# Performance work log

Hardware: AMD Instinct MI355X
Metric: run time of the kernel (lower is better)

The kernel has to match this reference:

```python
import jax, jax.numpy as jnp
import numpy as np

N_USERS = 100000
M_ITEMS = 50000
EMBED = 64
N_LAYERS = 3
NNZ = 2400000
BATCH = 8192


def setup_inputs() -> dict:
    key = jax.random.key(0)
    ks = jax.random.split(key, 8)
    user = jax.random.randint(ks[0], (BATCH,), 0, N_USERS)
    item_i = jax.random.randint(ks[1], (BATCH,), 0, M_ITEMS)
    item_j = jax.random.randint(ks[2], (BATCH,), 0, M_ITEMS)
    timestamp = jax.random.uniform(ks[3], (BATCH,), dtype=jnp.float32)
    # symmetric bipartite edge list: user->item and item->user halves
    half = NNZ // 2
    u = jax.random.randint(ks[4], (half,), 0, N_USERS)
    it = jax.random.randint(ks[5], (half,), 0, M_ITEMS) + N_USERS
    edge_src = jnp.concatenate([u, it])
    edge_dst = jnp.concatenate([it, u])
    v = jax.random.uniform(ks[6], (half,), dtype=jnp.float32)
    edge_vals = jnp.concatenate([v, v])  # symmetric normalized weights
    embed_user_0 = jax.random.normal(ks[7], (N_USERS, EMBED), dtype=jnp.float32) * 0.1
    embed_item_0 = jax.random.normal(jax.random.fold_in(key, 99), (M_ITEMS, EMBED), dtype=jnp.float32) * 0.1
    return {
        'user': user, 'item_i': item_i, 'item_j': item_j,
        'timestamp': timestamp, 'split_idx': 0,
        'edge_src': edge_src, 'edge_dst': edge_dst, 'edge_vals': edge_vals,
        'embed_user_0': embed_user_0, 'embed_item_0': embed_item_0,
    }


def reference(user, item_i, item_j, timestamp, split_idx,
              edge_src, edge_dst, edge_vals, embed_user_0, embed_item_0):
    N = N_USERS + M_ITEMS
    # LightGCN propagation: mean over layer-0..n_layers embeddings
    all_emb = jnp.concatenate([embed_user_0, embed_item_0], axis=0)  # [N, D]
    emb = all_emb
    emb_sum = all_emb
    for _ in range(N_LAYERS):
        # sparse.mm(Graph, emb): gather source features along edges, scale, segment-reduce
        emb = jax.ops.segment_sum(edge_vals[:, None] * emb[edge_dst], edge_src,
                                  num_segments=N)
        emb_sum = emb_sum + emb
    light_out = emb_sum / (N_LAYERS + 1)
    embed_user = light_out[:N_USERS]
    embed_item = light_out[N_USERS:]

    ue = embed_user[user]          # [B, D]
    ie = embed_item[item_i]        # [B, D]
    je = embed_item[item_j]        # [B, D]
    prediction_i = jnp.sum(ue * ie, axis=-1)
    prediction_j = jnp.sum(ue * je, axis=-1)

    # reg_loss uses layer-0 embeddings gathered at the batch indices
    u0 = embed_user_0[user]
    i0 = embed_item_0[item_i]
    j0 = embed_item_0[item_j]
    reg_loss = 0.5 * (jnp.sum(u0 * u0) + jnp.sum(i0 * i0) + jnp.sum(j0 * j0)) / user.shape[0]
    return prediction_i, prediction_j, reg_loss
```

## Files before the change

### kernel.cpp

```cpp
#include <hip/hip_runtime.h>

#define N_USERS 100000
#define M_ITEMS 50000
#define NNODES  (N_USERS + M_ITEMS)
#define EMBED   64
#define N_LAYERS 3
#define BATCH   8192

#define NU_E ((size_t)N_USERS * EMBED)
#define NI_E ((size_t)M_ITEMS * EMBED)
#define NE   ((size_t)NNODES * EMBED)

#define NPB    256
#define NBUCK  ((NNODES + NPB - 1) / NPB)
#define PBLK   256
#define HBB_N  (NBUCK * PBLK)
#define DBINS  1024
#define NCH    256
#define CHUNK  ((NNODES + NCH - 1) / NCH)
#define HBN    (DBINS * NCH)
#define PRED_BLOCKS ((BATCH * 64) / 256)

typedef unsigned int uint;

static __device__ __forceinline__ ushort f2bf(float f) {
    uint u = __float_as_uint(f);
    return (ushort)((u + 0x7fffu + ((u >> 16) & 1u)) >> 16);
}
static __device__ __forceinline__ float bf_lo(uint u) { return __uint_as_float(u << 16); }
static __device__ __forceinline__ float bf_hi(uint u) { return __uint_as_float(u & 0xffff0000u); }
static __device__ __forceinline__ float bfs(ushort u) { return __uint_as_float((uint)u << 16); }

__global__ void init_emb(const float* __restrict__ eu, const float* __restrict__ ei,
                         ushort* __restrict__ E0) {
    size_t t = (size_t)blockIdx.x * blockDim.x + threadIdx.x;
    const size_t nu4 = NU_E / 4;
    const size_t n4  = NE / 4;
    if (t >= n4) return;
    float4 v = (t < nu4) ? ((const float4*)eu)[t] : ((const float4*)ei)[t - nu4];
    ((ushort4*)E0)[t] = make_ushort4(f2bf(v.x), f2bf(v.y), f2bf(v.z), f2bf(v.w));
}

__global__ void hist_pass(const int* __restrict__ src, int* __restrict__ Hbb,
                          int nnz, int tile) {
    __shared__ int h[NBUCK];
    for (int i = threadIdx.x; i < NBUCK; i += blockDim.x) h[i] = 0;
    __syncthreads();
    int base = blockIdx.x * tile;
    int end  = min(base + tile, nnz);
    for (int i = base + threadIdx.x; i < end; i += blockDim.x)
        atomicAdd(&h[src[i] >> 8], 1);
    __syncthreads();
    for (int i = threadIdx.x; i < NBUCK; i += blockDim.x)
        Hbb[i * PBLK + blockIdx.x] = h[i];
}

__global__ void scan_local(int* __restrict__ h, int* __restrict__ bsum, int n) {
    __shared__ int lds[256];
    const int tid = threadIdx.x;
    const int base = blockIdx.x * 1024 + tid * 4;
    int v[4]; int s = 0;
    #pragma unroll
    for (int c = 0; c < 4; ++c) { v[c] = (base + c < n) ? h[base + c] : 0; s += v[c]; }
    lds[tid] = s;
    __syncthreads();
    for (int off = 1; off < 256; off <<= 1) {
        int t = (tid >= off) ? lds[tid - off] : 0;
        __syncthreads();
        lds[tid] += t;
        __syncthreads();
    }
    if (tid == 255) bsum[blockIdx.x] = lds[255];
    int run = (tid > 0) ? lds[tid - 1] : 0;
    #pragma unroll
    for (int c = 0; c < 4; ++c) {
        int t = v[c];
        if (base + c < n) h[base + c] = run;
        run += t;
    }
}
__global__ void scan_bsums(int* __restrict__ bsum, int nblk) {
    __shared__ int lds[256];
    int tid = threadIdx.x;
    lds[tid] = (tid < nblk) ? bsum[tid] : 0;
    __syncthreads();
    for (int off = 1; off < 256; off <<= 1) {
        int t = (tid >= off) ? lds[tid - off] : 0;
        __syncthreads();
        lds[tid] += t;
        __syncthreads();
    }
    if (tid < nblk) bsum[tid] = (tid > 0) ? lds[tid - 1] : 0;
}
__global__ void scan_add(int* __restrict__ h, const int* __restrict__ bsum, int n) {
    int i = blockIdx.x * blockDim.x + threadIdx.x;
    if (i >= n) return;
    h[i] += bsum[i / 1024];
}

__global__ void partition2(const int* __restrict__ src, const int* __restrict__ dst,
                           const float* __restrict__ vals, const int* __restrict__ Hbb,
                           int2* __restrict__ ebuf, int nnz, int tile) {
    __shared__ int cur[NBUCK];
    for (int i = threadIdx.x; i < NBUCK; i += blockDim.x)
        cur[i] = Hbb[i * PBLK + blockIdx.x];
    __syncthreads();
    int base = blockIdx.x * tile;
    int end  = min(base + tile, nnz);
    for (int i = base + threadIdx.x; i < end; i += blockDim.x) {
        int s = src[i];
        int d = dst[i];
        float v = vals[i];
        if (d >= N_USERS) d -= N_USERS;
        int p = atomicAdd(&cur[s >> 8], 1);
        ebuf[p] = make_int2((s & 255) | (d << 8), __float_as_int(v));
    }
}

__global__ void bucket_sort(const int* __restrict__ Hbb, const int2* __restrict__ ebuf,
                            int* __restrict__ offs, int2* __restrict__ ep, int nnz) {
    __shared__ int cnt[256];
    __shared__ int sc[256];
    __shared__ int cur[256];
    int b   = blockIdx.x;
    int tid = threadIdx.x;
    int beg = Hbb[b * PBLK];
    int end = (b + 1 < NBUCK) ? Hbb[(b + 1) * PBLK] : nnz;
    if (tid < 256) cnt[tid] = 0;
    __syncthreads();
    for (int i = beg + tid; i < end; i += blockDim.x)
        atomicAdd(&cnt[ebuf[i].x & 255], 1);
    __syncthreads();
    if (tid < 256) sc[tid] = cnt[tid];
    __syncthreads();
    for (int off = 1; off < 256; off <<= 1) {
        int t = (tid >= off && tid < 256) ? sc[tid - off] : 0;
        __syncthreads();
        if (tid < 256) sc[tid] += t;
        __syncthreads();
    }
    if (tid < 256) {
        int nodeBase = beg + ((tid > 0) ? sc[tid - 1] : 0);
        int node = b * NPB + tid;
        if (node < NNODES) offs[node] = nodeBase;
        cur[tid] = nodeBase;
    }
    __syncthreads();
    for (int i = beg + tid; i < end; i += blockDim.x) {
        int2 e = ebuf[i];
        int p = atomicAdd(&cur[e.x & 255], 1);
        ep[p] = make_int2(e.x >> 8, e.y);
    }
    if (b == 0 && tid == 0) offs[NNODES] = nnz;
}

__global__ void deg_hist_blk(const int* __restrict__ offs, int* __restrict__ Hb) {
    __shared__ int h[DBINS];
    int blk = blockIdx.x;
    for (int i = threadIdx.x; i < DBINS; i += blockDim.x) h[i] = 0;
    __syncthreads();
    int base = blk * CHUNK, end = min(base + CHUNK, NNODES);
    for (int n = base + threadIdx.x; n < end; n += blockDim.x)
        atomicAdd(&h[min(offs[n + 1] - offs[n], DBINS - 1)], 1);
    __syncthreads();
    for (int i = threadIdx.x; i < DBINS; i += blockDim.x)
        Hb[i * NCH + blk] = h[i];
}
__global__ void deg_scatter_blk(const int* __restrict__ offs, const int* __restrict__ Hb,
                                int* __restrict__ perm) {
    __shared__ int cur[DBINS];
    int blk = blockIdx.x;
    for (int i = threadIdx.x; i < DBINS; i += blockDim.x)
        cur[i] = Hb[i * NCH + blk];
    __syncthreads();
    int base = blk * CHUNK, end = min(base + CHUNK, NNODES);
    for (int n = base + threadIdx.x; n < end; n += blockDim.x) {
        int d = min(offs[n + 1] - offs[n], DBINS - 1);
        int p = atomicAdd(&cur[d], 1);
        perm[p] = n;
    }
}

__global__ void gather_E(const int* __restrict__ offs, const int2* __restrict__ ep,
                         const int* __restrict__ perm,
                         const ushort* __restrict__ Eprev, ushort* __restrict__ Enext,
                         int nnz) {
    int t = blockIdx.x * blockDim.x + threadIdx.x;
    int wave = t >> 6;
    int lane = t & 63;
    int g = lane >> 3;
    int q = lane & 7;
    int ln = wave * 8 + g;
    bool valid = ln < NNODES;
    int node = valid ? perm[ln] : 0;
    int start = valid ? offs[node] : 0;
    int deg   = valid ? offs[node + 1] - start : 0;
    bool isUser = node < N_USERS;
    const uint4* other = (const uint4*)(Eprev + (isUser ? NU_E : 0));
    int lastIdx = min(max(start + deg - 1, 0), nnz - 1);

    int md = deg;
    #pragma unroll
    for (int off = 8; off <= 32; off <<= 1) md = max(md, __shfl_xor(md, off));

    float a0=0.f,a1=0.f,a2=0.f,a3=0.f,a4=0.f,a5=0.f,a6=0.f,a7=0.f;
    for (int k = 0; k < md; k += 8) {
        int2 e[8];
        uint4 r[8];
        #pragma unroll
        for (int c = 0; c < 8; ++c) {
            int idx = (k + c < deg) ? start + k + c : lastIdx;
            e[c] = ep[idx];
            if (k + c >= deg) e[c].y = 0;
        }
        #pragma unroll
        for (int c = 0; c < 8; ++c)
            r[c] = other[(size_t)e[c].x * 8 + q];
        #pragma unroll
        for (int c = 0; c < 8; ++c) {
            float v = __int_as_float(e[c].y);
            a0 = fmaf(v, bf_lo(r[c].x), a0);  a1 = fmaf(v, bf_hi(r[c].x), a1);
            a2 = fmaf(v, bf_lo(r[c].y), a2);  a3 = fmaf(v, bf_hi(r[c].y), a3);
            a4 = fmaf(v, bf_lo(r[c].z), a4);  a5 = fmaf(v, bf_hi(r[c].z), a5);
            a6 = fmaf(v, bf_lo(r[c].w), a6);  a7 = fmaf(v, bf_hi(r[c].w), a7);
        }
    }

    if (!valid) return;
    uint4 o;
    o.x = (uint)f2bf(a0) | ((uint)f2bf(a1) << 16);
    o.y = (uint)f2bf(a2) | ((uint)f2bf(a3) << 16);
    o.z = (uint)f2bf(a4) | ((uint)f2bf(a5) << 16);
    o.w = (uint)f2bf(a6) | ((uint)f2bf(a7) << 16);
    ((uint4*)Enext)[(size_t)node * 8 + q] = o;
}

__global__ void predict_kernel(const int* __restrict__ user, const int* __restrict__ item_i,
                               const int* __restrict__ item_j,
                               const ushort* __restrict__ E0, const ushort* __restrict__ E1,
                               const ushort* __restrict__ E2, const ushort* __restrict__ E3,
                               const float* __restrict__ eu0, const float* __restrict__ ei0,
                               float* __restrict__ out, float* __restrict__ rbuf) {
    __shared__ float rpart[4];
    int t = blockIdx.x * blockDim.x + threadIdx.x;
    int b = t >> 6;
    int d = t & 63;
    int wv = threadIdx.x >> 6;
    float pi = 0.f, pj = 0.f, r = 0.f;
    if (b < BATCH) {
        size_t ru = (size_t)user[b] * EMBED + d;
        size_t ri = ((size_t)N_USERS + item_i[b]) * EMBED + d;
        size_t rj = ((size_t)N_USERS + item_j[b]) * EMBED + d;
        float ue = bfs(E0[ru]) + bfs(E1[ru]) + bfs(E2[ru]) + bfs(E3[ru]);
        float ie = bfs(E0[ri]) + bfs(E1[ri]) + bfs(E2[ri]) + bfs(E3[ri]);
        float je = bfs(E0[rj]) + bfs(E1[rj]) + bfs(E2[rj]) + bfs(E3[rj]);
        pi = ue * ie;
        pj = ue * je;
        float u0 = eu0[(size_t)user[b] * EMBED + d];
        float i0 = ei0[(size_t)item_i[b] * EMBED + d];
        float j0 = ei0[(size_t)item_j[b] * EMBED + d];
        r = u0 * u0 + i0 * i0 + j0 * j0;
    }
    #pragma unroll
    for (int off = 32; off > 0; off >>= 1) {
        pi += __shfl_down(pi, off);
        pj += __shfl_down(pj, off);
        r  += __shfl_down(r,  off);
    }
    if (d == 0 && b < BATCH) {
        out[b]         = pi * (1.0f / 16.0f);
        out[BATCH + b] = pj * (1.0f / 16.0f);
        rpart[wv] = r;
    }
    __syncthreads();
    if (threadIdx.x == 0)
        rbuf[blockIdx.x] = rpart[0] + rpart[1] + rpart[2] + rpart[3];
}

__global__ void finalize_reg(const float* __restrict__ rbuf, float* __restrict__ out) {
    __shared__ float lds[4];
    int tid = threadIdx.x;
    float s = 0.f;
    for (int i = tid; i < PRED_BLOCKS; i += 256) s += rbuf[i];
    #pragma unroll
    for (int off = 32; off > 0; off >>= 1) s += __shfl_down(s, off);
    if ((tid & 63) == 0) lds[tid >> 6] = s;
    __syncthreads();
    if (tid == 0)
        out[2 * BATCH] = (lds[0] + lds[1] + lds[2] + lds[3]) * (0.5f / (float)BATCH);
}

extern "C" void kernel_launch(void* const* d_in, const int* in_sizes, int n_in,
                              void* d_out, int out_size, void* d_ws, size_t ws_size,
                              hipStream_t stream) {
    const int*   user      = (const int*)  d_in[0];
    const int*   item_i    = (const int*)  d_in[1];
    const int*   item_j    = (const int*)  d_in[2];
    const int*   edge_src  = (const int*)  d_in[5];
    const int*   edge_dst  = (const int*)  d_in[6];
    const float* edge_vals = (const float*)d_in[7];
    const float* eu0       = (const float*)d_in[8];
    const float* ei0       = (const float*)d_in[9];
    const int    nnz       = in_sizes[5];

    float* out = (float*)d_out;

    ushort* E0   = (ushort*)d_ws;
    ushort* E1   = E0 + NE;
    ushort* E2   = E1 + NE;
    ushort* E3   = E2 + NE;
    int2*   ep   = (int2*)(E3 + NE);
    int*    offs = (int*)(ep + nnz);
    int*    Hbb  = offs + NNODES + 2;
    int*    bs1  = Hbb + HBB_N;
    int*    Hb   = bs1 + 256;
    int*    bs2  = Hb + HBN;
    int*    perm = bs2 + 256;
    float*  rbuf = (float*)(perm + NNODES);
    int2*   ebuf = (int2*)E1;

    const int tile = (nnz + PBLK - 1) / PBLK;
    const int nblk1 = (HBB_N + 1023) / 1024;
    hist_pass<<<PBLK, 1024, 0, stream>>>(edge_src, Hbb, nnz, tile);
    scan_local<<<nblk1, 256, 0, stream>>>(Hbb, bs1, HBB_N);
    scan_bsums<<<1, 256, 0, stream>>>(bs1, nblk1);
    scan_add<<<(HBB_N + 1023) / 1024, 1024, 0, stream>>>(Hbb, bs1, HBB_N);
    partition2<<<PBLK, 1024, 0, stream>>>(edge_src, edge_dst, edge_vals,
                                          Hbb, ebuf, nnz, tile);
    bucket_sort<<<NBUCK, 1024, 0, stream>>>(Hbb, ebuf, offs, ep, nnz);

    deg_hist_blk<<<NCH, 256, 0, stream>>>(offs, Hb);
    scan_local<<<HBN / 1024, 256, 0, stream>>>(Hb, bs2, HBN);
    scan_bsums<<<1, 256, 0, stream>>>(bs2, HBN / 1024);
    scan_add<<<HBN / 1024, 1024, 0, stream>>>(Hb, bs2, HBN);
    deg_scatter_blk<<<NCH, 256, 0, stream>>>(offs, Hb, perm);

    init_emb<<<(int)((NE / 4 + 255) / 256), 256, 0, stream>>>(eu0, ei0, E0);

    const int gblocks = (int)((((NNODES + 7) / 8) * 64 + 255) / 256);
    gather_E<<<gblocks, 256, 0, stream>>>(offs, ep, perm, E0, E1, nnz);
    gather_E<<<gblocks, 256, 0, stream>>>(offs, ep, perm, E1, E2, nnz);
    gather_E<<<gblocks, 256, 0, stream>>>(offs, ep, perm, E2, E3, nnz);

    predict_kernel<<<PRED_BLOCKS, 256, 0, stream>>>(
        user, item_i, item_j, E0, E1, E2, E3, eu0, ei0, out, rbuf);
    finalize_reg<<<1, 256, 0, stream>>>(rbuf, out);
}
```

Before: 336.3 us.

## Fuse preprocessing kernels and build degree permutation inside bucket sort

Cuts the launch count. The embedding bf16 conversion is merged into the histogram kernel. The bsum scan is folded into the add pass. The global degree-sorting passes are replaced by a per-bucket local degree sort inside bucket_sort. The final reg-loss reduction becomes a last-block pattern with an atomic counter. The perm ordering is now only local within 256-node buckets and degrees are capped at 255, which may reduce load balance in gather_E.

```diff
diff --git a/kernel.cpp b/kernel.cpp
--- a/kernel.cpp
+++ b/kernel.cpp
@@ -15,10 +15,7 @@
 #define NBUCK  ((NNODES + NPB - 1) / NPB)
 #define PBLK   256
 #define HBB_N  (NBUCK * PBLK)
-#define DBINS  1024
-#define NCH    256
-#define CHUNK  ((NNODES + NCH - 1) / NCH)
-#define HBN    (DBINS * NCH)
+#define SCAN_NB ((HBB_N + 1023) / 1024)
 #define PRED_BLOCKS ((BATCH * 64) / 256)
 
 typedef unsigned int uint;
@@ -31,28 +28,30 @@
 static __device__ __forceinline__ float bf_hi(uint u) { return __uint_as_float(u & 0xffff0000u); }
 static __device__ __forceinline__ float bfs(ushort u) { return __uint_as_float((uint)u << 16); }
 
-__global__ void init_emb(const float* __restrict__ eu, const float* __restrict__ ei,
-                         ushort* __restrict__ E0) {
-    size_t t = (size_t)blockIdx.x * blockDim.x + threadIdx.x;
-    const size_t nu4 = NU_E / 4;
-    const size_t n4  = NE / 4;
-    if (t >= n4) return;
-    float4 v = (t < nu4) ? ((const float4*)eu)[t] : ((const float4*)ei)[t - nu4];
-    ((ushort4*)E0)[t] = make_ushort4(f2bf(v.x), f2bf(v.y), f2bf(v.z), f2bf(v.w));
-}
-
-__global__ void hist_pass(const int* __restrict__ src, int* __restrict__ Hbb,
-                          int nnz, int tile) {
+__global__ void init_and_hist(const float* __restrict__ eu, const float* __restrict__ ei,
+                              ushort* __restrict__ E0,
+                              const int* __restrict__ src, int* __restrict__ Hbb,
+                              int nnz, int tile, int* __restrict__ counter) {
     __shared__ int h[NBUCK];
-    for (int i = threadIdx.x; i < NBUCK; i += blockDim.x) h[i] = 0;
-    __syncthreads();
-    int base = blockIdx.x * tile;
-    int end  = min(base + tile, nnz);
-    for (int i = base + threadIdx.x; i < end; i += blockDim.x)
-        atomicAdd(&h[src[i] >> 8], 1);
-    __syncthreads();
-    for (int i = threadIdx.x; i < NBUCK; i += blockDim.x)
-        Hbb[i * PBLK + blockIdx.x] = h[i];
+    if (blockIdx.x < PBLK) {
+        for (int i = threadIdx.x; i < NBUCK; i += blockDim.x) h[i] = 0;
+        __syncthreads();
+        int base = blockIdx.x * tile;
+        int end  = min(base + tile, nnz);
+        for (int i = base + threadIdx.x; i < end; i += blockDim.x)
+            atomicAdd(&h[src[i] >> 8], 1);
+        __syncthreads();
+        for (int i = threadIdx.x; i < NBUCK; i += blockDim.x)
+            Hbb[i * PBLK + blockIdx.x] = h[i];
+        if (blockIdx.x == 0 && threadIdx.x == 0) *counter = 0;
+    } else {
+        size_t t = (size_t)(blockIdx.x - PBLK) * blockDim.x + threadIdx.x;
+        const size_t nu4 = NU_E / 4;
+        const size_t n4  = NE / 4;
+        if (t >= n4) return;
+        float4 v = (t < nu4) ? ((const float4*)eu)[t] : ((const float4*)ei)[t - nu4];
+        ((ushort4*)E0)[t] = make_ushort4(f2bf(v.x), f2bf(v.y), f2bf(v.z), f2bf(v.w));
+    }
 }
 
 __global__ void scan_local(int* __restrict__ h, int* __restrict__ bsum, int n) {
@@ -79,23 +78,22 @@
         run += t;
     }
 }
-__global__ void scan_bsums(int* __restrict__ bsum, int nblk) {
+
+__global__ void scan_add2(int* __restrict__ h, const int* __restrict__ bsum,
+                          int n, int nblk) {
     __shared__ int lds[256];
     int tid = threadIdx.x;
-    lds[tid] = (tid < nblk) ? bsum[tid] : 0;
+    if (tid < 256) lds[tid] = (tid < nblk) ? bsum[tid] : 0;
     __syncthreads();
     for (int off = 1; off < 256; off <<= 1) {
-        int t = (tid >= off) ? lds[tid - off] : 0;
-        __syncthreads();
-        lds[tid] += t;
-        __syncthreads();
-    }
-    if (tid < nblk) bsum[tid] = (tid > 0) ? lds[tid - 1] : 0;
-}
-__global__ void scan_add(int* __restrict__ h, const int* __restrict__ bsum, int n) {
-    int i = blockIdx.x * blockDim.x + threadIdx.x;
-    if (i >= n) return;
-    h[i] += bsum[i / 1024];
+        int t = (tid >= off && tid < 256) ? lds[tid - off] : 0;
+        __syncthreads();
+        if (tid < 256) lds[tid] += t;
+        __syncthreads();
+    }
+    int prefix = (blockIdx.x > 0) ? lds[blockIdx.x - 1] : 0;
+    int i = blockIdx.x * 1024 + tid;
+    if (i < n) h[i] += prefix;
 }
 
 __global__ void partition2(const int* __restrict__ src, const int* __restrict__ dst,
@@ -117,11 +115,13 @@
     }
 }
 
-__global__ void bucket_sort(const int* __restrict__ Hbb, const int2* __restrict__ ebuf,
-                            int* __restrict__ offs, int2* __restrict__ ep, int nnz) {
+__global__ void bucket_sort_perm(const int* __restrict__ Hbb, const int2* __restrict__ ebuf,
+                                 int* __restrict__ offs, int2* __restrict__ ep,
+                                 int* __restrict__ perm, int nnz) {
     __shared__ int cnt[256];
     __shared__ int sc[256];
     __shared__ int cur[256];
+    __shared__ int dsc[256];
     int b   = blockIdx.x;
     int tid = threadIdx.x;
     int beg = Hbb[b * PBLK];
@@ -151,34 +151,31 @@
         int p = atomicAdd(&cur[e.x & 255], 1);
         ep[p] = make_int2(e.x >> 8, e.y);
     }
+    __syncthreads();
+    if (tid < 256) sc[tid] = 0;
+    __syncthreads();
+    int nodeCount = min(NNODES - b * NPB, NPB);
+    int deg = 0;
+    if (tid < nodeCount) {
+        deg = min(cnt[tid], 255);
+        atomicAdd(&sc[deg], 1);
+    }
+    __syncthreads();
+    if (tid < 256) dsc[tid] = sc[tid];
+    __syncthreads();
+    for (int off = 1; off < 256; off <<= 1) {
+        int t = (tid >= off && tid < 256) ? dsc[tid - off] : 0;
+        __syncthreads();
+        if (tid < 256) dsc[tid] += t;
+        __syncthreads();
+    }
+    if (tid < 256) cur[tid] = b * NPB + ((tid > 0) ? dsc[tid - 1] : 0);
+    __syncthreads();
+    if (tid < nodeCount) {
+        int rank = atomicAdd(&cur[deg], 1);
+        perm[rank] = b * NPB + tid;
+    }
     if (b == 0 && tid == 0) offs[NNODES] = nnz;
-}
-
-__global__ void deg_hist_blk(const int* __restrict__ offs, int* __restrict__ Hb) {
-    __shared__ int h[DBINS];
-    int blk = blockIdx.x;
-    for (int i = threadIdx.x; i < DBINS; i += blockDim.x) h[i] = 0;
-    __syncthreads();
-    int base = blk * CHUNK, end = min(base + CHUNK, NNODES);
-    for (int n = base + threadIdx.x; n < end; n += blockDim.x)
-        atomicAdd(&h[min(offs[n + 1] - offs[n], DBINS - 1)], 1);
-    __syncthreads();
-    for (int i = threadIdx.x; i < DBINS; i += blockDim.x)
-        Hb[i * NCH + blk] = h[i];
-}
-__global__ void deg_scatter_blk(const int* __restrict__ offs, const int* __restrict__ Hb,
-                                int* __restrict__ perm) {
-    __shared__ int cur[DBINS];
-    int blk = blockIdx.x;
-    for (int i = threadIdx.x; i < DBINS; i += blockDim.x)
-        cur[i] = Hb[i * NCH + blk];
-    __syncthreads();
-    int base = blk * CHUNK, end = min(base + CHUNK, NNODES);
-    for (int n = base + threadIdx.x; n < end; n += blockDim.x) {
-        int d = min(offs[n + 1] - offs[n], DBINS - 1);
-        int p = atomicAdd(&cur[d], 1);
-        perm[p] = n;
-    }
 }
 
 __global__ void gather_E(const int* __restrict__ offs, const int2* __restrict__ ep,
@@ -235,13 +232,15 @@
     ((uint4*)Enext)[(size_t)node * 8 + q] = o;
 }
 
-__global__ void predict_kernel(const int* __restrict__ user, const int* __restrict__ item_i,
-                               const int* __restrict__ item_j,
-                               const ushort* __restrict__ E0, const ushort* __restrict__ E1,
-                               const ushort* __restrict__ E2, const ushort* __restrict__ E3,
-                               const float* __restrict__ eu0, const float* __restrict__ ei0,
-                               float* __restrict__ out, float* __restrict__ rbuf) {
+__global__ void predict_fused(const int* __restrict__ user, const int* __restrict__ item_i,
+                              const int* __restrict__ item_j,
+                              const ushort* __restrict__ E0, const ushort* __restrict__ E1,
+                              const ushort* __restrict__ E2, const ushort* __restrict__ E3,
+                              const float* __restrict__ eu0, const float* __restrict__ ei0,
+                              float* __restrict__ out, float* __restrict__ rbuf,
+                              int* __restrict__ counter) {
     __shared__ float rpart[4];
+    __shared__ int isLast;
     int t = blockIdx.x * blockDim.x + threadIdx.x;
     int b = t >> 6;
     int d = t & 63;
@@ -273,21 +272,25 @@
         rpart[wv] = r;
     }
     __syncthreads();
-    if (threadIdx.x == 0)
-        rbuf[blockIdx.x] = rpart[0] + rpart[1] + rpart[2] + rpart[3];
-}
-
-__global__ void finalize_reg(const float* __restrict__ rbuf, float* __restrict__ out) {
-    __shared__ float lds[4];
-    int tid = threadIdx.x;
-    float s = 0.f;
-    for (int i = tid; i < PRED_BLOCKS; i += 256) s += rbuf[i];
-    #pragma unroll
-    for (int off = 32; off > 0; off >>= 1) s += __shfl_down(s, off);
-    if ((tid & 63) == 0) lds[tid >> 6] = s;
-    __syncthreads();
-    if (tid == 0)
-        out[2 * BATCH] = (lds[0] + lds[1] + lds[2] + lds[3]) * (0.5f / (float)BATCH);
+    if (threadIdx.x == 0) {
+        float bs = rpart[0] + rpart[1] + rpart[2] + rpart[3];
+        atomicExch(&rbuf[blockIdx.x], bs);
+        __threadfence();
+        isLast = (atomicAdd(counter, 1) == (int)gridDim.x - 1) ? 1 : 0;
+    }
+    __syncthreads();
+    if (isLast) {
+        float s = 0.f;
+        for (int i = threadIdx.x; i < PRED_BLOCKS; i += 256)
+            s += atomicAdd(&rbuf[i], 0.0f);
+        #pragma unroll
+        for (int off = 32; off > 0; off >>= 1) s += __shfl_down(s, off);
+        if ((threadIdx.x & 63) == 0) rpart[threadIdx.x >> 6] = s;
+        __syncthreads();
+        if (threadIdx.x == 0)
+            out[2 * BATCH] = (rpart[0] + rpart[1] + rpart[2] + rpart[3])
+                             * (0.5f / (float)BATCH);
+    }
 }
 
 extern "C" void kernel_launch(void* const* d_in, const int* in_sizes, int n_in,
@@ -312,37 +315,26 @@
     int2*   ep   = (int2*)(E3 + NE);
     int*    offs = (int*)(ep + nnz);
     int*    Hbb  = offs + NNODES + 2;
-    int*    bs1  = Hbb + HBB_N;
-    int*    Hb   = bs1 + 256;
-    int*    bs2  = Hb + HBN;
-    int*    perm = bs2 + 256;
+    int*    bsum = Hbb + HBB_N;
+    int*    perm = bsum + 256;
     float*  rbuf = (float*)(perm + NNODES);
+    int*    counter = (int*)(rbuf + PRED_BLOCKS);
     int2*   ebuf = (int2*)E1;
 
     const int tile = (nnz + PBLK - 1) / PBLK;
-    const int nblk1 = (HBB_N + 1023) / 1024;
-    hist_pass<<<PBLK, 1024, 0, stream>>>(edge_src, Hbb, nnz, tile);
-    scan_local<<<nblk1, 256, 0, stream>>>(Hbb, bs1, HBB_N);
-    scan_bsums<<<1, 256, 0, stream>>>(bs1, nblk1);
-    scan_add<<<(HBB_N + 1023) / 1024, 1024, 0, stream>>>(Hbb, bs1, HBB_N);
+    const int initBlocks = (int)((NE / 4 + 1023) / 1024);
+
+    init_and_hist<<<PBLK + initBlocks, 1024, 0, stream>>>(
+        eu0, ei0, E0, edge_src, Hbb, nnz, tile, counter);
+    scan_local<<<SCAN_NB, 256, 0, stream>>>(Hbb, bsum, HBB_N);
+    scan_add2<<<SCAN_NB, 1024, 0, stream>>>(Hbb, bsum, HBB_N, SCAN_NB);
     partition2<<<PBLK, 1024, 0, stream>>>(edge_src, edge_dst, edge_vals,
                                           Hbb, ebuf, nnz, tile);
-    bucket_sort<<<NBUCK, 1024, 0, stream>>>(Hbb, ebuf, offs, ep, nnz);
-
-    deg_hist_blk<<<NCH, 256, 0, stream>>>(offs, Hb);
-    scan_local<<<HBN / 1024, 256, 0, stream>>>(Hb, bs2, HBN);
-    scan_bsums<<<1, 256, 0, stream>>>(bs2, HBN / 1024);
-    scan_add<<<HBN / 1024, 1024, 0, stream>>>(Hb, bs2, HBN);
-    deg_scatter_blk<<<NCH, 256, 0, stream>>>(offs, Hb, perm);
-
-    init_emb<<<(int)((NE / 4 + 255) / 256), 256, 0, stream>>>(eu0, ei0, E0);
-
+    bucket_sort_perm<<<NBUCK, 1024, 0, stream>>>(Hbb, ebuf, offs, ep, perm, nnz);
     const int gblocks = (int)((((NNODES + 7) / 8) * 64 + 255) / 256);
     gather_E<<<gblocks, 256, 0, stream>>>(offs, ep, perm, E0, E1, nnz);
     gather_E<<<gblocks, 256, 0, stream>>>(offs, ep, perm, E1, E2, nnz);
     gather_E<<<gblocks, 256, 0, stream>>>(offs, ep, perm, E2, E3, nnz);
-
-    predict_kernel<<<PRED_BLOCKS, 256, 0, stream>>>(
-        user, item_i, item_j, E0, E1, E2, E3, eu0, ei0, out, rbuf);
-    finalize_reg<<<1, 256, 0, stream>>>(rbuf, out);
-}
+    predict_fused<<<PRED_BLOCKS, 256, 0, stream>>>(
+        user, item_i, item_j, E0, E1, E2, E3, eu0, ei0, out, rbuf, counter);
+}
```

New measurement: 385.4 us. 1.15x slower.
